# Kernel tuning notes

Measured on AMD Instinct MI355X. Metric: run time of the kernel, lower is better.

Reference implementation:

```python
import jax, jax.numpy as jnp
import numpy as np
import math

D_MODEL = 1024
RANK = 64
N_COMPRESS = 16
N_KNOWLEDGE = 16384
KNOWLEDGE_K = 8
B, S = 2, 4096


def setup_inputs() -> dict:
    key = jax.random.key(0)
    k = jax.random.split(key, 5)
    return {
        "x": jax.random.normal(k[0], (B, S, D_MODEL), dtype=jnp.float32),
        "memory_weights": jax.random.uniform(k[1], (B, S, N_COMPRESS), dtype=jnp.float32),
        "compress_neurons": jax.random.normal(k[2], (N_COMPRESS, D_MODEL, RANK), dtype=jnp.float32) * 0.02,
        "knowledge_K": jax.random.normal(k[3], (N_KNOWLEDGE, RANK), dtype=jnp.float32) * 0.02,
        "knowledge_V": jax.random.normal(k[4], (N_KNOWLEDGE, D_MODEL), dtype=jnp.float32) * 0.02,
    }


def reference(x, memory_weights, compress_neurons, knowledge_K, knowledge_V):
    # Reassociated contraction: avoids the (B,S,D,rank) intermediate of the
    # original torch code. tmp: [B,S,n_compress,rank] then weight by routing.
    # Q[b,s,r] = sum_n sum_d memory_weights[b,s,n] * x[b,s,d] * compress_neurons[n,d,r]
    Q = jnp.einsum('bsd,ndr,bsn->bsr', x, compress_neurons, memory_weights,
                   optimize=True)
    # knowledge_rank == rank, so query_proj is None
    scores = Q @ knowledge_K.T / math.sqrt(RANK)          # [B,S,N_KNOWLEDGE]
    topk_scores, topk_idx = jax.lax.top_k(scores, KNOWLEDGE_K)  # [B,S,k]
    weights = jax.nn.softmax(topk_scores, axis=-1)        # [B,S,k]
    selected_V = knowledge_V[topk_idx]                    # [B,S,k,D]
    output = jnp.einsum('bskd,bsk->bsd', selected_V, weights)
    return output, topk_idx, weights
```

## Files before the change

kernel.cpp:

```cpp
#include <hip/hip_runtime.h>
#include <hip/hip_bf16.h>

#define D_MODEL 1024
#define RANK 64
#define NCOMP 16
#define NKNOW 16384
#define TOPK 8
#define NTOK 8192
#define MAXG 48
#define NS 6

typedef __attribute__((ext_vector_type(4))) float f32x4;
typedef __attribute__((ext_vector_type(8))) short s16x8;
typedef unsigned short us;

static __device__ __forceinline__ us f2bf(float f) {
  union { float f; unsigned u; } v; v.f = f;
  unsigned r = v.u + 0x7FFFu + ((v.u >> 16) & 1u);
  return (us)(r >> 16);
}
static __device__ __forceinline__ float bf2f(us h) {
  union { unsigned u; float f; } v; v.u = ((unsigned)h) << 16;
  return v.f;
}

#define GLOAD16(g, l)                                                        \
  __builtin_amdgcn_global_load_lds(                                          \
      (const __attribute__((address_space(1))) void*)(g),                    \
      (__attribute__((address_space(3))) void*)(l), 16, 0, 0)

#define SPLIT3(f, h, m, l)                                                   \
  do {                                                                       \
    h = f2bf(f);                                                             \
    const float r1_ = (f) - bf2f(h);                                         \
    m = f2bf(r1_);                                                           \
    const float r2_ = r1_ - bf2f(m);                                         \
    l = f2bf(r2_);                                                           \
  } while (0)

__global__ __launch_bounds__(256) void k1cb3(const float* __restrict__ CN,
                                             us* __restrict__ Bh,
                                             us* __restrict__ Bm,
                                             us* __restrict__ Bl) {
  __shared__ float tile[64][65];
  const int n = blockIdx.x >> 4, dt = blockIdx.x & 15;
  const int tid = threadIdx.x;
  {
    const int d = tid >> 2, rc = (tid & 3) * 16;
    const float* p = CN + ((size_t)n * 1024 + dt * 64 + d) * 64 + rc;
#pragma unroll
    for (int e = 0; e < 16; e += 4) {
      const f32x4 v = *(const f32x4*)(p + e);
      tile[d][rc + e]     = v[0];
      tile[d][rc + e + 1] = v[1];
      tile[d][rc + e + 2] = v[2];
      tile[d][rc + e + 3] = v[3];
    }
  }
  __syncthreads();
  {
    const int r = tid >> 2, dc = (tid & 3) * 16;
    s16x8 oh[2], om[2], ol[2];
#pragma unroll
    for (int g = 0; g < 2; g++)
#pragma unroll
      for (int e = 0; e < 8; e++) {
        const float v = tile[dc + g * 8 + e][r];
        us h, m, l;
        SPLIT3(v, h, m, l);
        oh[g][e] = (short)h; om[g][e] = (short)m; ol[g][e] = (short)l;
      }
    const size_t base = (size_t)(n * 64 + r) * 1024 + dt * 64 + dc;
#pragma unroll
    for (int g = 0; g < 2; g++) {
      *(s16x8*)(Bh + base + g * 8) = oh[g];
      *(s16x8*)(Bm + base + g * 8) = om[g];
      *(s16x8*)(Bl + base + g * 8) = ol[g];
    }
  }
}

__global__ __launch_bounds__(256) void k1m3(const float* __restrict__ X,
                                            const us* __restrict__ Bh,
                                            const us* __restrict__ Bm,
                                            const us* __restrict__ Bl,
                                            float* __restrict__ T) {
  __shared__ us As[3][4][128][8];
  __shared__ us Bs[2][3][4][128][8];
  const int tid = threadIdx.x;
  const int w = tid >> 6, lane = tid & 63;
  const int wr = w >> 1, wc = w & 1;
  const int l15 = lane & 15, kq = lane >> 4;
  const int by = blockIdx.x >> 3, bx = blockIdx.x & 7;
  const int row0 = by * 128, col0 = bx * 128;

  const int sr = tid & 127, sh = tid >> 7;
  const float* xp = X + (size_t)(row0 + sr) * 1024 + sh * 16;

  const us* bsrc0[3]; const us* bsrc1[3];
  int bs_s[3], bs_q[3];
#pragma unroll
  for (int i = 0; i < 3; i++) {
    const int p = w * 3 + i;
    const int s = p >> 2, q = p & 3;
    bs_s[i] = s; bs_q[i] = q;
    const us* base = (s == 0) ? Bh : (s == 1) ? Bm : Bl;
    bsrc0[i] = base + (size_t)(col0 + lane) * 1024 + q * 8;
    bsrc1[i] = base + (size_t)(col0 + 64 + lane) * 1024 + q * 8;
  }

  f32x4 accH[4][4] = {};
  f32x4 accC[4][4] = {};
  f32x4 xr[4];
  s16x8 creg[6];

#pragma unroll
  for (int i = 0; i < 3; i++) {
    GLOAD16(bsrc0[i], &Bs[0][bs_s[i]][bs_q[i]][0][0]);
    GLOAD16(bsrc1[i], &Bs[0][bs_s[i]][bs_q[i]][64][0]);
  }
#pragma unroll
  for (int g = 0; g < 4; g++) xr[g] = *(const f32x4*)(xp + g * 4);
#pragma unroll
  for (int g = 0; g < 4; g++)
#pragma unroll
    for (int e = 0; e < 4; e++) {
      us h, m, l;
      SPLIT3(xr[g][e], h, m, l);
      const int c = (g * 4 + e) >> 3, e8 = (g * 4 + e) & 7;
      creg[c][e8] = (short)h; creg[2 + c][e8] = (short)m; creg[4 + c][e8] = (short)l;
    }

  for (int kk = 0; kk < 32; ++kk) {
    const int cur = kk & 1;
    *(s16x8*)&As[0][sh * 2][sr][0]     = creg[0];
    *(s16x8*)&As[0][sh * 2 + 1][sr][0] = creg[1];
    *(s16x8*)&As[1][sh * 2][sr][0]     = creg[2];
    *(s16x8*)&As[1][sh * 2 + 1][sr][0] = creg[3];
    *(s16x8*)&As[2][sh * 2][sr][0]     = creg[4];
    *(s16x8*)&As[2][sh * 2 + 1][sr][0] = creg[5];
    __syncthreads();

    if (kk + 1 < 32) {
      const int ko = (kk + 1) * 32;
#pragma unroll
      for (int i = 0; i < 3; i++) {
        GLOAD16(bsrc0[i] + ko, &Bs[cur ^ 1][bs_s[i]][bs_q[i]][0][0]);
        GLOAD16(bsrc1[i] + ko, &Bs[cur ^ 1][bs_s[i]][bs_q[i]][64][0]);
      }
#pragma unroll
      for (int g = 0; g < 4; g++) xr[g] = *(const f32x4*)(xp + ko + g * 4);
    }

#define PROD(sa, sb, ACC)                                                     \
    do {                                                                      \
      s16x8 af[4];                                                            \
      _Pragma("unroll")                                                       \
      for (int mm = 0; mm < 4; mm++)                                          \
        af[mm] = *(const s16x8*)&As[sa][kq][wr * 64 + mm * 16 + l15][0];      \
      _Pragma("unroll")                                                       \
      for (int nn = 0; nn < 4; nn++) {                                        \
        const s16x8 bfr =                                                     \
            *(const s16x8*)&Bs[cur][sb][kq][wc * 64 + nn * 16 + l15][0];      \
        _Pragma("unroll")                                                     \
        for (int mm = 0; mm < 4; mm++)                                        \
          ACC[mm][nn] = __builtin_amdgcn_mfma_f32_16x16x32_bf16(              \
              af[mm], bfr, ACC[mm][nn], 0, 0, 0);                             \
      }                                                                       \
    } while (0)

    PROD(0, 0, accH);
    PROD(0, 1, accC); PROD(1, 0, accC); PROD(0, 2, accC);
    PROD(2, 0, accC); PROD(1, 1, accC);
#undef PROD

    if (kk + 1 < 32) {
#pragma unroll
      for (int g = 0; g < 4; g++)
#pragma unroll
        for (int e = 0; e < 4; e++) {
          us h, m, l;
          SPLIT3(xr[g][e], h, m, l);
          const int c = (g * 4 + e) >> 3, e8 = (g * 4 + e) & 7;
          creg[c][e8] = (short)h; creg[2 + c][e8] = (short)m;
          creg[4 + c][e8] = (short)l;
        }
    }
    __syncthreads();
  }

#pragma unroll
  for (int mm = 0; mm < 4; mm++)
#pragma unroll
    for (int nn = 0; nn < 4; nn++)
#pragma unroll
      for (int r = 0; r < 4; r++)
        T[(size_t)(row0 + wr * 64 + mm * 16 + kq * 4 + r) * 1024
          + col0 + wc * 64 + nn * 16 + l15] = accH[mm][nn][r] + accC[mm][nn][r];
}

__global__ __launch_bounds__(256) void k1b_weight(const float* __restrict__ T,
                                                  const float* __restrict__ MW,
                                                  float* __restrict__ Qf,
                                                  us* __restrict__ Qb) {
  const int gid = blockIdx.x * 256 + threadIdx.x;
  const int tok = gid >> 6, r = gid & 63;
  float q = 0.f;
#pragma unroll
  for (int n = 0; n < 16; n++)
    q = fmaf(MW[tok * 16 + n], T[(size_t)tok * 1024 + n * 64 + r], q);
  Qf[gid] = q;
  Qb[gid] = f2bf(q);
}

__global__ __launch_bounds__(256) void k1c_cvt(const float* __restrict__ Kf,
                                               us* __restrict__ Kb) {
  const int gid = blockIdx.x * 256 + threadIdx.x;
  f32x4 v = *(const f32x4*)(Kf + (size_t)gid * 4);
  us o0 = f2bf(v[0]), o1 = f2bf(v[1]), o2 = f2bf(v[2]), o3 = f2bf(v[3]);
  unsigned long long pack = (unsigned long long)o0 | ((unsigned long long)o1 << 16)
                          | ((unsigned long long)o2 << 32) | ((unsigned long long)o3 << 48);
  *(unsigned long long*)(Kb + (size_t)gid * 4) = pack;
}

__global__ __launch_bounds__(256) void k2s_screen(
    const us* __restrict__ Qb, const us* __restrict__ Kb,
    us* __restrict__ GM) {
  __shared__ us sh[4][32][136];
  const int tid = threadIdx.x;
  const int wv = tid >> 6, lane = tid & 63;
  const int gw = blockIdx.x * 4 + wv;
  const int tg = gw >> 4;
  const int jsl = gw & 15;
  const int tb = tg * 32;
  const int myTok = lane & 15;
  const int slice = lane >> 4;

  const s16x8 bfa0 = *(const s16x8*)(Qb + (size_t)(tb + myTok) * 64 + slice * 8);
  const s16x8 bfa1 = *(const s16x8*)(Qb + (size_t)(tb + myTok) * 64 + 32 + slice * 8);
  const s16x8 bfb0 = *(const s16x8*)(Qb + (size_t)(tb + 16 + myTok) * 64 + slice * 8);
  const s16x8 bfb1 = *(const s16x8*)(Qb + (size_t)(tb + 16 + myTok) * 64 + 32 + slice * 8);

  const int j0 = jsl * 1024;
  const us* ap0 = Kb + (size_t)(j0 + myTok) * 64 + slice * 8;
  s16x8 af0 = *(const s16x8*)(ap0);
  s16x8 af1 = *(const s16x8*)(ap0 + 32);
  const bool writer = (slice & 1) == 0;
  const int sub = slice >> 1;

  for (int tt = 0; tt < 64; ++tt) {
    f32x4 ca = {0.f, 0.f, 0.f, 0.f};
    f32x4 cb = {0.f, 0.f, 0.f, 0.f};
    ca = __builtin_amdgcn_mfma_f32_16x16x32_bf16(af0, bfa0, ca, 0, 0, 0);
    cb = __builtin_amdgcn_mfma_f32_16x16x32_bf16(af0, bfb0, cb, 0, 0, 0);
    ca = __builtin_amdgcn_mfma_f32_16x16x32_bf16(af1, bfa1, ca, 0, 0, 0);
    cb = __builtin_amdgcn_mfma_f32_16x16x32_bf16(af1, bfb1, cb, 0, 0, 0);
    if (tt + 1 < 64) {
      const us* ap = ap0 + (size_t)(tt + 1) * 16 * 64;
      af0 = *(const s16x8*)(ap);
      af1 = *(const s16x8*)(ap + 32);
    }
    const float gma4 = fmaxf(fmaxf(ca[0], ca[1]), fmaxf(ca[2], ca[3]));
    const float gma8 = fmaxf(gma4, __shfl_xor(gma4, 16));
    const float gmb4 = fmaxf(fmaxf(cb[0], cb[1]), fmaxf(cb[2], cb[3]));
    const float gmb8 = fmaxf(gmb4, __shfl_xor(gmb4, 16));
    if (writer) {
      sh[wv][myTok][2 * tt + sub] = f2bf(gma8);
      sh[wv][16 + myTok][2 * tt + sub] = f2bf(gmb8);
    }
  }
  __syncthreads();
  {
    const int t = lane >> 1;
    const int half = (lane & 1) * 64;
    us* orow = GM + (size_t)(tb + t) * 2048 + jsl * 128 + half;
#pragma unroll
    for (int ch = 0; ch < 8; ch++)
      *(s16x8*)(orow + ch * 8) = *(const s16x8*)&sh[wv][t][half + ch * 8];
  }
}

__global__ __launch_bounds__(256) void k2b_select(
    const float* __restrict__ Qf, const float* __restrict__ Kf,
    const float* __restrict__ V, const us* __restrict__ GM,
    float* __restrict__ out, float* __restrict__ out_idx,
    float* __restrict__ out_w) {
  __shared__ float qsh[4][64];
  __shared__ int csh[4][MAXG];
  __shared__ int scnt[4];
  const int tid = threadIdx.x;
  const int wv = tid >> 6, lane = tid & 63;
  const int tok = blockIdx.x * 4 + wv;

  if (lane == 0) scnt[wv] = 0;
  qsh[wv][lane] = Qf[(size_t)tok * 64 + lane];

  unsigned long long gv[8];
  const unsigned long long* gmp =
      (const unsigned long long*)(GM + (size_t)tok * 2048);
#pragma unroll
  for (int i = 0; i < 8; i++) gv[i] = gmp[i * 64 + lane];

  float lm = -1e30f;
#pragma unroll
  for (int i = 0; i < 8; i++)
#pragma unroll
    for (int e = 0; e < 4; e++)
      lm = fmaxf(lm, bf2f((us)(gv[i] >> (e * 16))));

  float v = lm, m8 = -1e30f;
#pragma unroll
  for (int e = 0; e < 8; e++) {
    float m = v;
#pragma unroll
    for (int d = 1; d < 64; d <<= 1) m = fmaxf(m, __shfl_xor(m, d));
    m8 = m;
    if (e < 7) v = (v == m) ? -1e30f : v;
  }
  const float thr = m8 - 0.04f;

#pragma unroll
  for (int i = 0; i < 8; i++) {
#pragma unroll
    for (int e = 0; e < 4; e++) {
      const float g = bf2f((us)(gv[i] >> (e * 16)));
      if (g >= thr) {
        const int s = atomicAdd(&scnt[wv], 1);
        if (s < MAXG) csh[wv][s] = i * 256 + lane * 4 + e;
      }
    }
  }
  int ng = scnt[wv];
  if (ng > MAXG) ng = MAXG;
  const int nj = ng * 8;

  float scR[NS]; int jR[NS];
#pragma unroll
  for (int s = 0; s < NS; s++) {
    scR[s] = -1e30f; jR[s] = 0x7fffffff;
    if (s * 64 < nj) {
      const int ci = s * 64 + lane;
      if (ci < nj) {
        const int j = csh[wv][ci >> 3] * 8 + (ci & 7);
        const float* kp = Kf + (size_t)j * 64;
        float acc = 0.f;
#pragma unroll
        for (int k = 0; k < 64; k += 4) {
          const f32x4 qv = *(const f32x4*)&qsh[wv][k];
          const f32x4 kv = *(const f32x4*)(kp + k);
          acc = fmaf(qv[0], kv[0], acc);
          acc = fmaf(qv[1], kv[1], acc);
          acc = fmaf(qv[2], kv[2], acc);
          acc = fmaf(qv[3], kv[3], acc);
        }
        scR[s] = acc * 0.125f; jR[s] = j;
      }
    }
  }

  float wsv[8]; int wjv[8];
#pragma unroll
  for (int e = 0; e < 8; e++) {
    float ms = scR[0]; int mj = jR[0];
#pragma unroll
    for (int s = 1; s < NS; s++)
      if (scR[s] > ms || (scR[s] == ms && jR[s] < mj)) { ms = scR[s]; mj = jR[s]; }
#pragma unroll
    for (int d = 1; d < 64; d <<= 1) {
      const float rs = __shfl_xor(ms, d);
      const int rj = __shfl_xor(mj, d);
      if (rs > ms || (rs == ms && rj < mj)) { ms = rs; mj = rj; }
    }
    wsv[e] = ms; wjv[e] = mj;
#pragma unroll
    for (int s = 0; s < NS; s++)
      if (jR[s] == mj) { scR[s] = -1e30f; jR[s] = 0x7fffffff; }
  }

  const float m0 = wsv[0];
  float ex[8], sum = 0.f;
#pragma unroll
  for (int r = 0; r < 8; r++) { ex[r] = expf(wsv[r] - m0); sum += ex[r]; }
  const float inv = 1.f / sum;

  if (lane == 0) {
#pragma unroll
    for (int r = 0; r < 8; r++) {
      out_idx[(size_t)tok * 8 + r] = (float)wjv[r];
      out_w[(size_t)tok * 8 + r] = ex[r] * inv;
    }
  }

  f32x4 a0 = {0.f,0.f,0.f,0.f}, a1 = a0, a2 = a0, a3 = a0;
#pragma unroll
  for (int r = 0; r < 8; r++) {
    const float w = ex[r] * inv;
    const float* vp = V + (size_t)(wjv[r] & (NKNOW - 1)) * 1024 + lane * 16;
    const f32x4 v0 = *(const f32x4*)(vp);
    const f32x4 v1 = *(const f32x4*)(vp + 4);
    const f32x4 v2 = *(const f32x4*)(vp + 8);
    const f32x4 v3 = *(const f32x4*)(vp + 12);
    a0 += w * v0; a1 += w * v1; a2 += w * v2; a3 += w * v3;
  }
  float* op = out + (size_t)tok * 1024 + lane * 16;
  *(f32x4*)(op)      = a0;
  *(f32x4*)(op + 4)  = a1;
  *(f32x4*)(op + 8)  = a2;
  *(f32x4*)(op + 12) = a3;
}

extern "C" void kernel_launch(void* const* d_in, const int* in_sizes, int n_in,
                              void* d_out, int out_size, void* d_ws, size_t ws_size,
                              hipStream_t stream) {
  const float* x  = (const float*)d_in[0];
  const float* mw = (const float*)d_in[1];
  const float* cn = (const float*)d_in[2];
  const float* kK = (const float*)d_in[3];
  const float* kV = (const float*)d_in[4];

  float* out  = (float*)d_out;
  float* oidx = out + (size_t)NTOK * D_MODEL;
  float* ow   = oidx + (size_t)NTOK * TOPK;

  float* T   = (float*)d_ws;
  us* GM     = (us*)d_ws;
  float* Qf  = (float*)((char*)d_ws + 33554432);
  us* Qb     = (us*)((char*)d_ws + 35651584);
  us* Kb     = (us*)((char*)d_ws + 36700160);
  us* Bh     = (us*)((char*)d_ws + 38797312);
  us* Bm     = (us*)((char*)d_ws + 40894464);
  us* Bl     = (us*)((char*)d_ws + 42991616);

  k1cb3<<<256, 256, 0, stream>>>(cn, Bh, Bm, Bl);
  k1m3<<<512, 256, 0, stream>>>(x, Bh, Bm, Bl, T);
  k1b_weight<<<2048, 256, 0, stream>>>(T, mw, Qf, Qb);
  k1c_cvt<<<1024, 256, 0, stream>>>(kK, Kb);
  k2s_screen<<<1024, 256, 0, stream>>>(Qb, Kb, GM);
  k2b_select<<<2048, 256, 0, stream>>>(Qf, kK, kV, GM, out, oidx, ow);

  (void)in_sizes; (void)n_in; (void)out_size; (void)ws_size;
}
```

Measured before the change: 294.0 us.

## Merge K conversion into prep kernel, widen screen MFMA, split select and gather

The knowledge-K bf16 conversion is folded into the compress-neuron split kernel as extra blocks, which removes one launch. The screening kernel now processes two 16-row K tiles per iteration with four independent MFMA accumulators, so it runs half as many loop trips and has more independent matrix work in flight. The selection kernel is split so that the V gather and weighted sum run in their own kernel, reading indices and weights back from the output buffers. This adds a launch and an extra round trip of idx/weight data, in exchange for lower register and latency pressure in the selection kernel.

```diff
diff --git a/kernel.cpp b/kernel.cpp
--- a/kernel.cpp
+++ b/kernel.cpp
@@ -41,10 +41,21 @@
 __global__ __launch_bounds__(256) void k1cb3(const float* __restrict__ CN,
                                              us* __restrict__ Bh,
                                              us* __restrict__ Bm,
-                                             us* __restrict__ Bl) {
+                                             us* __restrict__ Bl,
+                                             const float* __restrict__ Kf,
+                                             us* __restrict__ Kb) {
   __shared__ float tile[64][65];
+  const int tid = threadIdx.x;
+  if (blockIdx.x >= 256) {
+    const int gid = (blockIdx.x - 256) * 256 + tid;
+    f32x4 v = *(const f32x4*)(Kf + (size_t)gid * 4);
+    us o0 = f2bf(v[0]), o1 = f2bf(v[1]), o2 = f2bf(v[2]), o3 = f2bf(v[3]);
+    unsigned long long pack = (unsigned long long)o0 | ((unsigned long long)o1 << 16)
+                            | ((unsigned long long)o2 << 32) | ((unsigned long long)o3 << 48);
+    *(unsigned long long*)(Kb + (size_t)gid * 4) = pack;
+    return;
+  }
   const int n = blockIdx.x >> 4, dt = blockIdx.x & 15;
-  const int tid = threadIdx.x;
   {
     const int d = tid >> 2, rc = (tid & 3) * 16;
     const float* p = CN + ((size_t)n * 1024 + dt * 64 + d) * 64 + rc;
@@ -213,16 +224,6 @@
   Qb[gid] = f2bf(q);
 }
 
-__global__ __launch_bounds__(256) void k1c_cvt(const float* __restrict__ Kf,
-                                               us* __restrict__ Kb) {
-  const int gid = blockIdx.x * 256 + threadIdx.x;
-  f32x4 v = *(const f32x4*)(Kf + (size_t)gid * 4);
-  us o0 = f2bf(v[0]), o1 = f2bf(v[1]), o2 = f2bf(v[2]), o3 = f2bf(v[3]);
-  unsigned long long pack = (unsigned long long)o0 | ((unsigned long long)o1 << 16)
-                          | ((unsigned long long)o2 << 32) | ((unsigned long long)o3 << 48);
-  *(unsigned long long*)(Kb + (size_t)gid * 4) = pack;
-}
-
 __global__ __launch_bounds__(256) void k2s_screen(
     const us* __restrict__ Qb, const us* __restrict__ Kb,
     us* __restrict__ GM) {
@@ -243,30 +244,44 @@
 
   const int j0 = jsl * 1024;
   const us* ap0 = Kb + (size_t)(j0 + myTok) * 64 + slice * 8;
-  s16x8 af0 = *(const s16x8*)(ap0);
-  s16x8 af1 = *(const s16x8*)(ap0 + 32);
+  s16x8 afA0 = *(const s16x8*)(ap0);
+  s16x8 afA1 = *(const s16x8*)(ap0 + 32);
+  s16x8 afB0 = *(const s16x8*)(ap0 + 32 * 1024);
+  s16x8 afB1 = *(const s16x8*)(ap0 + 32 * 1024 + 32);
   const bool writer = (slice & 1) == 0;
   const int sub = slice >> 1;
 
-  for (int tt = 0; tt < 64; ++tt) {
-    f32x4 ca = {0.f, 0.f, 0.f, 0.f};
-    f32x4 cb = {0.f, 0.f, 0.f, 0.f};
-    ca = __builtin_amdgcn_mfma_f32_16x16x32_bf16(af0, bfa0, ca, 0, 0, 0);
-    cb = __builtin_amdgcn_mfma_f32_16x16x32_bf16(af0, bfb0, cb, 0, 0, 0);
-    ca = __builtin_amdgcn_mfma_f32_16x16x32_bf16(af1, bfa1, ca, 0, 0, 0);
-    cb = __builtin_amdgcn_mfma_f32_16x16x32_bf16(af1, bfb1, cb, 0, 0, 0);
-    if (tt + 1 < 64) {
-      const us* ap = ap0 + (size_t)(tt + 1) * 16 * 64;
-      af0 = *(const s16x8*)(ap);
-      af1 = *(const s16x8*)(ap + 32);
-    }
-    const float gma4 = fmaxf(fmaxf(ca[0], ca[1]), fmaxf(ca[2], ca[3]));
-    const float gma8 = fmaxf(gma4, __shfl_xor(gma4, 16));
-    const float gmb4 = fmaxf(fmaxf(cb[0], cb[1]), fmaxf(cb[2], cb[3]));
-    const float gmb8 = fmaxf(gmb4, __shfl_xor(gmb4, 16));
+  for (int tt = 0; tt < 32; ++tt) {
+    f32x4 ca = {0.f,0.f,0.f,0.f}, cb = ca, cc = ca, cd = ca;
+    ca = __builtin_amdgcn_mfma_f32_16x16x32_bf16(afA0, bfa0, ca, 0, 0, 0);
+    cb = __builtin_amdgcn_mfma_f32_16x16x32_bf16(afA0, bfb0, cb, 0, 0, 0);
+    cc = __builtin_amdgcn_mfma_f32_16x16x32_bf16(afB0, bfa0, cc, 0, 0, 0);
+    cd = __builtin_amdgcn_mfma_f32_16x16x32_bf16(afB0, bfb0, cd, 0, 0, 0);
+    ca = __builtin_amdgcn_mfma_f32_16x16x32_bf16(afA1, bfa1, ca, 0, 0, 0);
+    cb = __builtin_amdgcn_mfma_f32_16x16x32_bf16(afA1, bfb1, cb, 0, 0, 0);
+    cc = __builtin_amdgcn_mfma_f32_16x16x32_bf16(afB1, bfa1, cc, 0, 0, 0);
+    cd = __builtin_amdgcn_mfma_f32_16x16x32_bf16(afB1, bfb1, cd, 0, 0, 0);
+    if (tt + 1 < 32) {
+      const us* apA = ap0 + (size_t)(tt + 1) * 1024;
+      const us* apB = apA + 32 * 1024;
+      afA0 = *(const s16x8*)(apA);
+      afA1 = *(const s16x8*)(apA + 32);
+      afB0 = *(const s16x8*)(apB);
+      afB1 = *(const s16x8*)(apB + 32);
+    }
+    const float ga4 = fmaxf(fmaxf(ca[0], ca[1]), fmaxf(ca[2], ca[3]));
+    const float ga8 = fmaxf(ga4, __shfl_xor(ga4, 16));
+    const float gb4 = fmaxf(fmaxf(cb[0], cb[1]), fmaxf(cb[2], cb[3]));
+    const float gb8 = fmaxf(gb4, __shfl_xor(gb4, 16));
+    const float gc4 = fmaxf(fmaxf(cc[0], cc[1]), fmaxf(cc[2], cc[3]));
+    const float gc8 = fmaxf(gc4, __shfl_xor(gc4, 16));
+    const float gd4 = fmaxf(fmaxf(cd[0], cd[1]), fmaxf(cd[2], cd[3]));
+    const float gd8 = fmaxf(gd4, __shfl_xor(gd4, 16));
     if (writer) {
-      sh[wv][myTok][2 * tt + sub] = f2bf(gma8);
-      sh[wv][16 + myTok][2 * tt + sub] = f2bf(gmb8);
+      sh[wv][myTok][2 * tt + sub]           = f2bf(ga8);
+      sh[wv][16 + myTok][2 * tt + sub]      = f2bf(gb8);
+      sh[wv][myTok][64 + 2 * tt + sub]      = f2bf(gc8);
+      sh[wv][16 + myTok][64 + 2 * tt + sub] = f2bf(gd8);
     }
   }
   __syncthreads();
@@ -280,11 +295,10 @@
   }
 }
 
-__global__ __launch_bounds__(256) void k2b_select(
+__global__ __launch_bounds__(256) void k2b_sel(
     const float* __restrict__ Qf, const float* __restrict__ Kf,
-    const float* __restrict__ V, const us* __restrict__ GM,
-    float* __restrict__ out, float* __restrict__ out_idx,
-    float* __restrict__ out_w) {
+    const us* __restrict__ GM,
+    float* __restrict__ out_idx, float* __restrict__ out_w) {
   __shared__ float qsh[4][64];
   __shared__ int csh[4][MAXG];
   __shared__ int scnt[4];
@@ -390,12 +404,27 @@
       out_w[(size_t)tok * 8 + r] = ex[r] * inv;
     }
   }
+}
+
+__global__ __launch_bounds__(256) void k2g_gather(
+    const float* __restrict__ V, const float* __restrict__ out_idx,
+    const float* __restrict__ out_w, float* __restrict__ out) {
+  const int tid = threadIdx.x;
+  const int wv = tid >> 6, lane = tid & 63;
+  const int tok = blockIdx.x * 4 + wv;
+
+  int jv[8]; float wv8[8];
+#pragma unroll
+  for (int r = 0; r < 8; r++) {
+    jv[r] = ((int)out_idx[(size_t)tok * 8 + r]) & (NKNOW - 1);
+    wv8[r] = out_w[(size_t)tok * 8 + r];
+  }
 
   f32x4 a0 = {0.f,0.f,0.f,0.f}, a1 = a0, a2 = a0, a3 = a0;
 #pragma unroll
   for (int r = 0; r < 8; r++) {
-    const float w = ex[r] * inv;
-    const float* vp = V + (size_t)(wjv[r] & (NKNOW - 1)) * 1024 + lane * 16;
+    const float w = wv8[r];
+    const float* vp = V + (size_t)jv[r] * 1024 + lane * 16;
     const f32x4 v0 = *(const f32x4*)(vp);
     const f32x4 v1 = *(const f32x4*)(vp + 4);
     const f32x4 v2 = *(const f32x4*)(vp + 8);
@@ -431,12 +460,12 @@
   us* Bm     = (us*)((char*)d_ws + 40894464);
   us* Bl     = (us*)((char*)d_ws + 42991616);
 
-  k1cb3<<<256, 256, 0, stream>>>(cn, Bh, Bm, Bl);
+  k1cb3<<<1280, 256, 0, stream>>>(cn, Bh, Bm, Bl, kK, Kb);
   k1m3<<<512, 256, 0, stream>>>(x, Bh, Bm, Bl, T);
   k1b_weight<<<2048, 256, 0, stream>>>(T, mw, Qf, Qb);
-  k1c_cvt<<<1024, 256, 0, stream>>>(kK, Kb);
   k2s_screen<<<1024, 256, 0, stream>>>(Qb, Kb, GM);
-  k2b_select<<<2048, 256, 0, stream>>>(Qf, kK, kV, GM, out, oidx, ow);
+  k2b_sel<<<2048, 256, 0, stream>>>(Qf, kK, GM, oidx, ow);
+  k2g_gather<<<2048, 256, 0, stream>>>(kV, oidx, ow, out);
 
   (void)in_sizes; (void)n_in; (void)out_size; (void)ws_size;
 }
```

New measurement: 295.6 us. Within noise of the previous version (+0.6%).
